# Kernel optimization log

Measured on AMD Instinct MI355X. Metric: run time of the kernel, lower is better.

## Reference

```python
import jax, jax.numpy as jnp
import numpy as np
from jax import lax

DN = ('NCHW', 'OIHW', 'NCHW')
MAX_CLAMP = 0.75


def conv_s2(x, w):
    # kernel 9x9, stride 2, padding 4, no bias
    return lax.conv_general_dilated(x, w, window_strides=(2, 2),
                                    padding=[(4, 4), (4, 4)],
                                    dimension_numbers=DN)


def setup_inputs() -> dict:
    key = jax.random.key(0)
    k_x, k1, k2, k3, k4 = jax.random.split(key, 5)
    num_maps = 32
    x = jax.random.normal(k_x, (1024, 2, 128, 128), dtype=jnp.float32)
    # PyTorch Conv2d default init ~ U(-1/sqrt(fan_in), 1/sqrt(fan_in)); scale similarly
    w1 = jax.random.normal(k1, (8, 2, 9, 9), dtype=jnp.float32) * (1.0 / np.sqrt(2 * 81))
    w2 = jax.random.normal(k2, (8, 8, 9, 9), dtype=jnp.float32) * (1.0 / np.sqrt(8 * 81))
    w3 = jax.random.normal(k3, (num_maps, 8, 9, 9), dtype=jnp.float32) * (1.0 / np.sqrt(8 * 81))
    wfc = jax.random.normal(k4, (2, num_maps), dtype=jnp.float32) * (1.0 / np.sqrt(num_maps))
    return {"x": x, "w1": w1, "w2": w2, "w3": w3, "wfc": wfc}


def reference(x, w1, w2, w3, wfc):
    conv1 = jax.nn.relu(conv_s2(x, w1))                  # [B, 8, 64, 64]
    conv2 = jax.nn.relu(conv_s2(conv1, w2))              # [B, 8, 32, 32]
    conv3 = jax.nn.relu(conv_s2(conv2, w3))              # [B, M, 16, 16]
    # per-channel max over 16x16 spatial, threshold at 0.75*max, zero below
    maps_max = jnp.max(conv3, axis=(2, 3), keepdims=True) * MAX_CLAMP
    conv3_masked = jnp.where(conv3 < maps_max, 0.0, conv3)
    pool = jnp.mean(conv3_masked, axis=(2, 3))           # AvgPool2d((16,16)) -> [B, M]
    logits = pool @ wfc.T                                # Linear(M, 2, bias=False)
    y = jax.nn.log_softmax(logits, axis=1)
    return (y, conv3_masked, pool)
```

## Files before the change

### kernel.cpp

```cpp
#include <hip/hip_runtime.h>
#include <hip/hip_bf16.h>
#include <math.h>


#define RELU(v) fmaxf((v), 0.0f)

__device__ __forceinline__ int swzq(int q) { return q ^ ((q >> 3) & 7); }

__global__ __launch_bounds__(256) void conv1_kernel(
    const float* __restrict__ x, const float* __restrict__ w1,
    float* __restrict__ out1) {
  __shared__ float sIn[39 * 164];
  __shared__ float sW[81 * 8];
  const int tid = threadIdx.x;
  const int b = blockIdx.x >> 2;
  const int oy0 = (blockIdx.x & 3) << 4;
  const int iy0 = 2 * oy0 - 4;
  const float* xb = x + (size_t)b * (2 * 128 * 128);

  const int ty = tid >> 4;
  const int tx = tid & 15;
  int roff[4];
#pragma unroll
  for (int q = 0; q < 4; q++) roff[q] = swzq(2 * tx + q) * 4;

  float acc[8][4];
#pragma unroll
  for (int co = 0; co < 8; co++)
#pragma unroll
    for (int i = 0; i < 4; i++) acc[co][i] = 0.f;

#pragma unroll 1
  for (int ci = 0; ci < 2; ci++) {
    __syncthreads();
    for (int i = tid; i < 648; i += 256) {
      int co = i / 81;
      int rem = i - co * 81;
      sW[rem * 8 + co] = w1[co * 162 + ci * 81 + rem];
    }
    for (int i = tid; i < 39 * 34; i += 256) {
      int r = i / 34;
      int seg = i - r * 34;
      int gy = iy0 + r;
      float4 v = make_float4(0.f, 0.f, 0.f, 0.f);
      if (gy >= 0 && gy < 128 && seg >= 1 && seg <= 32)
        v = *reinterpret_cast<const float4*>(xb + (ci * 128 + gy) * 128 + (seg * 4 - 4));
      *reinterpret_cast<float4*>(&sIn[r * 164 + swzq(seg) * 4]) = v;
    }
    __syncthreads();
#pragma unroll 1
    for (int ky = 0; ky < 9; ky++) {
      const int rb = (2 * ty + ky) * 164;
      float xv[16];
#pragma unroll
      for (int q = 0; q < 4; q++) {
        float4 t = *reinterpret_cast<const float4*>(&sIn[rb + roff[q]]);
        xv[4 * q + 0] = t.x; xv[4 * q + 1] = t.y;
        xv[4 * q + 2] = t.z; xv[4 * q + 3] = t.w;
      }
      const float* wrow = &sW[ky * 72];
#pragma unroll
      for (int kx = 0; kx < 9; kx++) {
        float4 wa = *reinterpret_cast<const float4*>(wrow + kx * 8);
        float4 wb = *reinterpret_cast<const float4*>(wrow + kx * 8 + 4);
        float wv[8] = {wa.x, wa.y, wa.z, wa.w, wb.x, wb.y, wb.z, wb.w};
#pragma unroll
        for (int co = 0; co < 8; co++)
#pragma unroll
          for (int i = 0; i < 4; i++)
            acc[co][i] = fmaf(xv[kx + 2 * i], wv[co], acc[co][i]);
      }
    }
  }
  const int oy = oy0 + ty;
  float* ob = out1 + (size_t)b * (8 * 64 * 64);
#pragma unroll
  for (int co = 0; co < 8; co++) {
    float4 v = make_float4(RELU(acc[co][0]), RELU(acc[co][1]),
                           RELU(acc[co][2]), RELU(acc[co][3]));
    *reinterpret_cast<float4*>(ob + (co * 64 + oy) * 64 + 4 * tx) = v;
  }
}

__global__ __launch_bounds__(256) void conv2_kernel(
    const float* __restrict__ in, const float* __restrict__ w2,
    float* __restrict__ out2) {
  __shared__ float sIn[71 * 84];
  __shared__ float sW[81 * 8];
  const int tid = threadIdx.x;
  const int b = blockIdx.x;
  const float* ib = in + (size_t)b * (8 * 64 * 64);
  const int oy = tid >> 3;
  const int tx = tid & 7;
  int roff[4];
#pragma unroll
  for (int q = 0; q < 4; q++) roff[q] = swzq(2 * tx + q) * 4;

  float acc[8][4];
#pragma unroll
  for (int co = 0; co < 8; co++)
#pragma unroll
    for (int i = 0; i < 4; i++) acc[co][i] = 0.f;

#pragma unroll 1
  for (int ci = 0; ci < 8; ci++) {
    __syncthreads();
    for (int i = tid; i < 648; i += 256) {
      int co = i / 81;
      int rem = i - co * 81;
      sW[rem * 8 + co] = w2[co * 648 + ci * 81 + rem];
    }
    for (int i = tid; i < 71 * 18; i += 256) {
      int r = i / 18;
      int seg = i - r * 18;
      int gy = r - 4;
      float4 v = make_float4(0.f, 0.f, 0.f, 0.f);
      if (gy >= 0 && gy < 64 && seg >= 1 && seg <= 16)
        v = *reinterpret_cast<const float4*>(ib + (ci * 64 + gy) * 64 + (seg * 4 - 4));
      *reinterpret_cast<float4*>(&sIn[r * 84 + swzq(seg) * 4]) = v;
    }
    __syncthreads();
#pragma unroll 1
    for (int ky = 0; ky < 9; ky++) {
      const int rb = (2 * oy + ky) * 84;
      float xv[16];
#pragma unroll
      for (int q = 0; q < 4; q++) {
        float4 t = *reinterpret_cast<const float4*>(&sIn[rb + roff[q]]);
        xv[4 * q + 0] = t.x; xv[4 * q + 1] = t.y;
        xv[4 * q + 2] = t.z; xv[4 * q + 3] = t.w;
      }
      const float* wrow = &sW[ky * 72];
#pragma unroll
      for (int kx = 0; kx < 9; kx++) {
        float4 wa = *reinterpret_cast<const float4*>(wrow + kx * 8);
        float4 wb = *reinterpret_cast<const float4*>(wrow + kx * 8 + 4);
        float wv[8] = {wa.x, wa.y, wa.z, wa.w, wb.x, wb.y, wb.z, wb.w};
#pragma unroll
        for (int co = 0; co < 8; co++)
#pragma unroll
          for (int i = 0; i < 4; i++)
            acc[co][i] = fmaf(xv[kx + 2 * i], wv[co], acc[co][i]);
      }
    }
  }
  float* ob = out2 + (size_t)b * (8 * 32 * 32);
#pragma unroll
  for (int co = 0; co < 8; co++) {
    float4 v = make_float4(RELU(acc[co][0]), RELU(acc[co][1]),
                           RELU(acc[co][2]), RELU(acc[co][3]));
    *reinterpret_cast<float4*>(ob + (co * 32 + oy) * 32 + 4 * tx) = v;
  }
}

__global__ __launch_bounds__(256) void conv3_kernel(
    const float* __restrict__ in, const float* __restrict__ w3,
    float* __restrict__ masked_out, float* __restrict__ pool) {
  __shared__ float sIn[2 * 39 * 40];
  __shared__ float sW[2 * 81 * 8];
  __shared__ float sMax[8];
  const int tid = threadIdx.x;
  const int b = blockIdx.x >> 2;
  const int co0 = (blockIdx.x & 3) << 3;
  const float* ib = in + (size_t)b * (8 * 32 * 32);

  const int oy = tid >> 4;
  const int ox = tid & 15;
  float acc[8];
#pragma unroll
  for (int co = 0; co < 8; co++) acc[co] = 0.f;

#pragma unroll 1
  for (int cg = 0; cg < 4; cg++) {
    __syncthreads();
    for (int i = tid; i < 1296; i += 256) {
      int cop = i / 162;
      int r2 = i - cop * 162;
      sW[r2 * 8 + cop] = w3[(co0 + cop) * 648 + cg * 162 + r2];
    }
    for (int i = tid; i < 2 * 39 * 10; i += 256) {
      int c = i / 390;
      int rem = i - c * 390;
      int r = rem / 10;
      int seg = rem - r * 10;
      int gy = r - 4;
      float4 v = make_float4(0.f, 0.f, 0.f, 0.f);
      if (gy >= 0 && gy < 32 && seg >= 1 && seg <= 8)
        v = *reinterpret_cast<const float4*>(ib + ((2 * cg + c) * 32 + gy) * 32 + (seg * 4 - 4));
      *reinterpret_cast<float4*>(&sIn[(c * 39 + r) * 40 + seg * 4]) = v;
    }
    __syncthreads();
#pragma unroll 1
    for (int c = 0; c < 2; c++) {
#pragma unroll 1
      for (int ky = 0; ky < 9; ky++) {
        const int r = 2 * oy + ky;
        const float* row = &sIn[(c * 39 + r) * 40 + 2 * ox];
        float xv[10];
#pragma unroll
        for (int q = 0; q < 5; q++) {
          float2 t = *reinterpret_cast<const float2*>(row + 2 * q);
          xv[2 * q + 0] = t.x; xv[2 * q + 1] = t.y;
        }
        const float* wrow = &sW[(c * 81 + ky * 9) * 8];
#pragma unroll
        for (int kx = 0; kx < 9; kx++) {
          float4 wa = *reinterpret_cast<const float4*>(wrow + kx * 8);
          float4 wb = *reinterpret_cast<const float4*>(wrow + kx * 8 + 4);
          float wv[8] = {wa.x, wa.y, wa.z, wa.w, wb.x, wb.y, wb.z, wb.w};
#pragma unroll
          for (int co = 0; co < 8; co++)
            acc[co] = fmaf(xv[kx], wv[co], acc[co]);
        }
      }
    }
  }
#pragma unroll
  for (int co = 0; co < 8; co++) acc[co] = RELU(acc[co]);

  __syncthreads();
  float* red = sIn;
#pragma unroll
  for (int co = 0; co < 8; co++) red[co * 256 + tid] = acc[co];
  __syncthreads();
  {
    const int co = tid >> 5;
    const int j = tid & 31;
    float m = 0.f;
    for (int p = j; p < 256; p += 32) m = fmaxf(m, red[co * 256 + p]);
#pragma unroll
    for (int k = 16; k >= 1; k >>= 1) m = fmaxf(m, __shfl_xor(m, k));
    if (j == 0) sMax[co] = m * 0.75f;
  }
  __syncthreads();

  float* mb = masked_out + ((size_t)b * 32 + co0) * 256 + tid;
#pragma unroll
  for (int co = 0; co < 8; co++) {
    float v = acc[co];
    v = (v < sMax[co]) ? 0.f : v;
    red[co * 256 + tid] = v;
    mb[co * 256] = v;
  }
  __syncthreads();
  {
    const int co = tid >> 5;
    const int j = tid & 31;
    float s = 0.f;
    for (int p = j; p < 256; p += 32) s += red[co * 256 + p];
#pragma unroll
    for (int k = 16; k >= 1; k >>= 1) s += __shfl_xor(s, k);
    if (j == 0) pool[(size_t)b * 32 + co0 + co] = s * (1.0f / 256.0f);
  }
}

__global__ __launch_bounds__(256) void head_kernel(
    const float* __restrict__ pool, const float* __restrict__ wfc,
    float* __restrict__ y) {
  __shared__ float sw[64];
  if (threadIdx.x < 64) sw[threadIdx.x] = wfc[threadIdx.x];
  __syncthreads();
  const int b = blockIdx.x * 256 + threadIdx.x;
  const float* pb = pool + (size_t)b * 32;
  float l0 = 0.f, l1 = 0.f;
#pragma unroll
  for (int q = 0; q < 8; q++) {
    float4 p = *reinterpret_cast<const float4*>(pb + 4 * q);
    l0 += p.x * sw[4 * q + 0] + p.y * sw[4 * q + 1] +
          p.z * sw[4 * q + 2] + p.w * sw[4 * q + 3];
    l1 += p.x * sw[32 + 4 * q + 0] + p.y * sw[32 + 4 * q + 1] +
          p.z * sw[32 + 4 * q + 2] + p.w * sw[32 + 4 * q + 3];
  }
  float m = fmaxf(l0, l1);
  float lz = logf(expf(l0 - m) + expf(l1 - m)) + m;
  float2 out = make_float2(l0 - lz, l1 - lz);
  *reinterpret_cast<float2*>(y + 2 * b) = out;
}

extern "C" void kernel_launch(void* const* d_in, const int* in_sizes, int n_in,
                              void* d_out, int out_size, void* d_ws, size_t ws_size,
                              hipStream_t stream) {
  const float* x   = (const float*)d_in[0];
  const float* w1  = (const float*)d_in[1];
  const float* w2  = (const float*)d_in[2];
  const float* w3  = (const float*)d_in[3];
  const float* wfc = (const float*)d_in[4];

  float* out = (float*)d_out;
  float* y      = out;
  float* masked = out + 2048;
  float* pool   = out + 2048 + 1024 * 32 * 256;

  float* c1 = (float*)d_ws;
  float* c2 = c1 + (size_t)1024 * 8 * 64 * 64;

  conv1_kernel<<<4096, 256, 0, stream>>>(x, w1, c1);
  conv2_kernel<<<1024, 256, 0, stream>>>(c1, w2, c2);
  conv3_kernel<<<4096, 256, 0, stream>>>(c2, w3, masked, pool);
  head_kernel<<<4, 256, 0, stream>>>(pool, wfc, y);
}
```

Measured before the change: 644.2 us.

## Read conv weights via uniform scalar loads and retile conv3 per wave

```diff
diff --git a/kernel.cpp b/kernel.cpp
--- a/kernel.cpp
+++ b/kernel.cpp
@@ -11,7 +11,6 @@
     const float* __restrict__ x, const float* __restrict__ w1,
     float* __restrict__ out1) {
   __shared__ float sIn[39 * 164];
-  __shared__ float sW[81 * 8];
   const int tid = threadIdx.x;
   const int b = blockIdx.x >> 2;
   const int oy0 = (blockIdx.x & 3) << 4;
@@ -33,11 +32,6 @@
 #pragma unroll 1
   for (int ci = 0; ci < 2; ci++) {
     __syncthreads();
-    for (int i = tid; i < 648; i += 256) {
-      int co = i / 81;
-      int rem = i - co * 81;
-      sW[rem * 8 + co] = w1[co * 162 + ci * 81 + rem];
-    }
     for (int i = tid; i < 39 * 34; i += 256) {
       int r = i / 34;
       int seg = i - r * 34;
@@ -58,17 +52,17 @@
         xv[4 * q + 0] = t.x; xv[4 * q + 1] = t.y;
         xv[4 * q + 2] = t.z; xv[4 * q + 3] = t.w;
       }
-      const float* wrow = &sW[ky * 72];
-#pragma unroll
-      for (int kx = 0; kx < 9; kx++) {
-        float4 wa = *reinterpret_cast<const float4*>(wrow + kx * 8);
-        float4 wb = *reinterpret_cast<const float4*>(wrow + kx * 8 + 4);
-        float wv[8] = {wa.x, wa.y, wa.z, wa.w, wb.x, wb.y, wb.z, wb.w};
-#pragma unroll
-        for (int co = 0; co < 8; co++)
+#pragma unroll
+      for (int co = 0; co < 8; co++) {
+        const float* wr = w1 + (co * 2 + ci) * 81 + ky * 9;
+        float w[9];
+#pragma unroll
+        for (int k = 0; k < 9; k++) w[k] = wr[k];
+#pragma unroll
+        for (int kx = 0; kx < 9; kx++)
 #pragma unroll
           for (int i = 0; i < 4; i++)
-            acc[co][i] = fmaf(xv[kx + 2 * i], wv[co], acc[co][i]);
+            acc[co][i] = fmaf(xv[kx + 2 * i], w[kx], acc[co][i]);
       }
     }
   }
@@ -86,7 +80,6 @@
     const float* __restrict__ in, const float* __restrict__ w2,
     float* __restrict__ out2) {
   __shared__ float sIn[71 * 84];
-  __shared__ float sW[81 * 8];
   const int tid = threadIdx.x;
   const int b = blockIdx.x;
   const float* ib = in + (size_t)b * (8 * 64 * 64);
@@ -105,11 +98,6 @@
 #pragma unroll 1
   for (int ci = 0; ci < 8; ci++) {
     __syncthreads();
-    for (int i = tid; i < 648; i += 256) {
-      int co = i / 81;
-      int rem = i - co * 81;
-      sW[rem * 8 + co] = w2[co * 648 + ci * 81 + rem];
-    }
     for (int i = tid; i < 71 * 18; i += 256) {
       int r = i / 18;
       int seg = i - r * 18;
@@ -130,17 +118,17 @@
         xv[4 * q + 0] = t.x; xv[4 * q + 1] = t.y;
         xv[4 * q + 2] = t.z; xv[4 * q + 3] = t.w;
       }
-      const float* wrow = &sW[ky * 72];
-#pragma unroll
-      for (int kx = 0; kx < 9; kx++) {
-        float4 wa = *reinterpret_cast<const float4*>(wrow + kx * 8);
-        float4 wb = *reinterpret_cast<const float4*>(wrow + kx * 8 + 4);
-        float wv[8] = {wa.x, wa.y, wa.z, wa.w, wb.x, wb.y, wb.z, wb.w};
-#pragma unroll
-        for (int co = 0; co < 8; co++)
+#pragma unroll
+      for (int co = 0; co < 8; co++) {
+        const float* wr = w2 + (co * 8 + ci) * 81 + ky * 9;
+        float w[9];
+#pragma unroll
+        for (int k = 0; k < 9; k++) w[k] = wr[k];
+#pragma unroll
+        for (int kx = 0; kx < 9; kx++)
 #pragma unroll
           for (int i = 0; i < 4; i++)
-            acc[co][i] = fmaf(xv[kx + 2 * i], wv[co], acc[co][i]);
+            acc[co][i] = fmaf(xv[kx + 2 * i], w[kx], acc[co][i]);
       }
     }
   }
@@ -156,28 +144,24 @@
 __global__ __launch_bounds__(256) void conv3_kernel(
     const float* __restrict__ in, const float* __restrict__ w3,
     float* __restrict__ masked_out, float* __restrict__ pool) {
-  __shared__ float sIn[2 * 39 * 40];
-  __shared__ float sW[2 * 81 * 8];
-  __shared__ float sMax[8];
+  __shared__ float sIn[2 * 39 * 44];
   const int tid = threadIdx.x;
-  const int b = blockIdx.x >> 2;
-  const int co0 = (blockIdx.x & 3) << 3;
+  const int b = blockIdx.x;
+  const int co0 = __builtin_amdgcn_readfirstlane(tid >> 6) * 8;
+  const int p = tid & 63;
+  const int oy = p >> 2;
+  const int oxg = p & 3;
   const float* ib = in + (size_t)b * (8 * 32 * 32);
 
-  const int oy = tid >> 4;
-  const int ox = tid & 15;
-  float acc[8];
-#pragma unroll
-  for (int co = 0; co < 8; co++) acc[co] = 0.f;
+  float acc[8][4];
+#pragma unroll
+  for (int co = 0; co < 8; co++)
+#pragma unroll
+    for (int i = 0; i < 4; i++) acc[co][i] = 0.f;
 
 #pragma unroll 1
   for (int cg = 0; cg < 4; cg++) {
     __syncthreads();
-    for (int i = tid; i < 1296; i += 256) {
-      int cop = i / 162;
-      int r2 = i - cop * 162;
-      sW[r2 * 8 + cop] = w3[(co0 + cop) * 648 + cg * 162 + r2];
-    }
     for (int i = tid; i < 2 * 39 * 10; i += 256) {
       int c = i / 390;
       int rem = i - c * 390;
@@ -187,70 +171,68 @@
       float4 v = make_float4(0.f, 0.f, 0.f, 0.f);
       if (gy >= 0 && gy < 32 && seg >= 1 && seg <= 8)
         v = *reinterpret_cast<const float4*>(ib + ((2 * cg + c) * 32 + gy) * 32 + (seg * 4 - 4));
-      *reinterpret_cast<float4*>(&sIn[(c * 39 + r) * 40 + seg * 4]) = v;
+      *reinterpret_cast<float4*>(&sIn[(c * 39 + r) * 44 + seg * 4]) = v;
     }
     __syncthreads();
 #pragma unroll 1
     for (int c = 0; c < 2; c++) {
+      const int ci = 2 * cg + c;
 #pragma unroll 1
       for (int ky = 0; ky < 9; ky++) {
-        const int r = 2 * oy + ky;
-        const float* row = &sIn[(c * 39 + r) * 40 + 2 * ox];
-        float xv[10];
-#pragma unroll
-        for (int q = 0; q < 5; q++) {
-          float2 t = *reinterpret_cast<const float2*>(row + 2 * q);
-          xv[2 * q + 0] = t.x; xv[2 * q + 1] = t.y;
+        const int rb = (c * 39 + 2 * oy + ky) * 44;
+        float xv[16];
+#pragma unroll
+        for (int q = 0; q < 4; q++) {
+          float4 t = *reinterpret_cast<const float4*>(&sIn[rb + (2 * oxg + q) * 4]);
+          xv[4 * q + 0] = t.x; xv[4 * q + 1] = t.y;
+          xv[4 * q + 2] = t.z; xv[4 * q + 3] = t.w;
         }
-        const float* wrow = &sW[(c * 81 + ky * 9) * 8];
-#pragma unroll
-        for (int kx = 0; kx < 9; kx++) {
-          float4 wa = *reinterpret_cast<const float4*>(wrow + kx * 8);
-          float4 wb = *reinterpret_cast<const float4*>(wrow + kx * 8 + 4);
-          float wv[8] = {wa.x, wa.y, wa.z, wa.w, wb.x, wb.y, wb.z, wb.w};
-#pragma unroll
-          for (int co = 0; co < 8; co++)
-            acc[co] = fmaf(xv[kx], wv[co], acc[co]);
+#pragma unroll
+        for (int co = 0; co < 8; co++) {
+          const float* wr = w3 + ((co0 + co) * 8 + ci) * 81 + ky * 9;
+          float w[9];
+#pragma unroll
+          for (int k = 0; k < 9; k++) w[k] = wr[k];
+#pragma unroll
+          for (int kx = 0; kx < 9; kx++)
+#pragma unroll
+            for (int i = 0; i < 4; i++)
+              acc[co][i] = fmaf(xv[kx + 2 * i], w[kx], acc[co][i]);
         }
       }
     }
   }
-#pragma unroll
-  for (int co = 0; co < 8; co++) acc[co] = RELU(acc[co]);
-
-  __syncthreads();
-  float* red = sIn;
-#pragma unroll
-  for (int co = 0; co < 8; co++) red[co * 256 + tid] = acc[co];
-  __syncthreads();
-  {
-    const int co = tid >> 5;
-    const int j = tid & 31;
-    float m = 0.f;
-    for (int p = j; p < 256; p += 32) m = fmaxf(m, red[co * 256 + p]);
-#pragma unroll
-    for (int k = 16; k >= 1; k >>= 1) m = fmaxf(m, __shfl_xor(m, k));
-    if (j == 0) sMax[co] = m * 0.75f;
-  }
-  __syncthreads();
-
-  float* mb = masked_out + ((size_t)b * 32 + co0) * 256 + tid;
-#pragma unroll
-  for (int co = 0; co < 8; co++) {
-    float v = acc[co];
-    v = (v < sMax[co]) ? 0.f : v;
-    red[co * 256 + tid] = v;
-    mb[co * 256] = v;
-  }
-  __syncthreads();
-  {
-    const int co = tid >> 5;
-    const int j = tid & 31;
-    float s = 0.f;
-    for (int p = j; p < 256; p += 32) s += red[co * 256 + p];
-#pragma unroll
-    for (int k = 16; k >= 1; k >>= 1) s += __shfl_xor(s, k);
-    if (j == 0) pool[(size_t)b * 32 + co0 + co] = s * (1.0f / 256.0f);
+
+  float thr[8];
+#pragma unroll
+  for (int co = 0; co < 8; co++) {
+#pragma unroll
+    for (int i = 0; i < 4; i++) acc[co][i] = RELU(acc[co][i]);
+    float m = fmaxf(fmaxf(acc[co][0], acc[co][1]), fmaxf(acc[co][2], acc[co][3]));
+#pragma unroll
+    for (int k = 32; k >= 1; k >>= 1) m = fmaxf(m, __shfl_xor(m, k));
+    thr[co] = m * 0.75f;
+  }
+
+  float* mb = masked_out + ((size_t)b * 32 + co0) * 256 + 4 * p;
+  float sum[8];
+#pragma unroll
+  for (int co = 0; co < 8; co++) {
+    float4 v;
+    v.x = (acc[co][0] < thr[co]) ? 0.f : acc[co][0];
+    v.y = (acc[co][1] < thr[co]) ? 0.f : acc[co][1];
+    v.z = (acc[co][2] < thr[co]) ? 0.f : acc[co][2];
+    v.w = (acc[co][3] < thr[co]) ? 0.f : acc[co][3];
+    *reinterpret_cast<float4*>(mb + co * 256) = v;
+    float s = v.x + v.y + v.z + v.w;
+#pragma unroll
+    for (int k = 32; k >= 1; k >>= 1) s += __shfl_xor(s, k);
+    sum[co] = s;
+  }
+  if (p == 0) {
+#pragma unroll
+    for (int co = 0; co < 8; co++)
+      pool[(size_t)b * 32 + co0 + co] = sum[co] * (1.0f / 256.0f);
   }
 }
 
@@ -296,6 +278,6 @@
 
   conv1_kernel<<<4096, 256, 0, stream>>>(x, w1, c1);
   conv2_kernel<<<1024, 256, 0, stream>>>(c1, w2, c2);
-  conv3_kernel<<<4096, 256, 0, stream>>>(c2, w3, masked, pool);
+  conv3_kernel<<<1024, 256, 0, stream>>>(c2, w3, masked, pool);
   head_kernel<<<4, 256, 0, stream>>>(pool, wfc, y);
 }
```

Measured after the change: 517.8 us. -19.6%, faster.
